# Kernel optimization log

Hardware: AMD Instinct MI355X
Metric: run time of the kernel (lower is better)

Reference implementation:

```python
import jax, jax.numpy as jnp
import numpy as np

B, TQ, TK, D, R, H = 4, 2048, 2048, 1024, 64, 512
TAU_BASE, ASTRO_DECAY = 1.0, 0.95


def setup_inputs() -> dict:
    key = jax.random.key(0)
    ks = jax.random.split(key, 20)
    xav = lambda k, din, dout: jax.random.uniform(k, (din, dout), jnp.float32, -1.0, 1.0) * np.sqrt(6.0 / (din + dout))
    inp = {
        'q_in': jax.random.normal(ks[0], (B, TQ, D), jnp.float32),
        'k_in': jax.random.normal(ks[1], (B, TK, D), jnp.float32),
        'v_in': jax.random.normal(ks[2], (B, TK, D), jnp.float32),
        'astrocyte_state': jnp.zeros((B,), jnp.float32),
        'Wq': xav(ks[3], D, D), 'bq': jnp.zeros((D,), jnp.float32),
        'Wk': xav(ks[4], D, D), 'bk': jnp.zeros((D,), jnp.float32),
        'Wv': xav(ks[5], D, D), 'bv': jnp.zeros((D,), jnp.float32),
        'Wo': xav(ks[6], D, D), 'bo': jnp.zeros((D,), jnp.float32),
        # orthonormal role rows (R <= D): QR of a random D x R matrix, rows = Q^T
        'role_matrix': jnp.linalg.qr(jax.random.normal(ks[7], (D, R), jnp.float32))[0].T,
        'Wr1': xav(ks[8], D, H), 'br1': jnp.zeros((H,), jnp.float32),
        'Wr2': xav(ks[9], H, R),
        'astro_scale': jnp.ones((1,), jnp.float32),
    }
    return inp


def _l2norm(x, axis=-1, eps=1e-12):
    return x / jnp.clip(jnp.linalg.norm(x, axis=axis, keepdims=True), eps)


def _bind_vectors(a, b):
    # holographic (circular-convolution) binding via FFT along feature dim
    n = a.shape[-1]
    return jnp.fft.irfft(jnp.fft.rfft(a, axis=-1) * jnp.fft.rfft(b, axis=-1), n=n, axis=-1)


def _compute_surprise(Q):
    # per-token surprise: RMS-normalized L2 magnitude of projected queries -> (B, T_q)
    return jnp.linalg.norm(Q, axis=-1) / np.sqrt(Q.shape[-1])


def reference(q_in, k_in, v_in, astrocyte_state, Wq, bq, Wk, bk, Wv, bv, Wo, bo,
              role_matrix, Wr1, br1, Wr2, astro_scale):
    Q = q_in @ Wq + bq                      # (B,TQ,D)
    K = k_in @ Wk + bk                      # (B,TK,D)
    V = v_in @ Wv + bv                      # (B,TK,D)

    role_mat_norm = _l2norm(role_matrix)    # (R,D)
    role_logits = jax.nn.relu(K @ Wr1 + br1) @ Wr2          # (B,TK,R)
    role_weights = jax.nn.softmax(role_logits, axis=-1)
    role_vecs = role_weights @ role_mat_norm                 # (B,TK,D)
    K_bound = _bind_vectors(K, role_vecs)                    # (B,TK,D)

    surprise = _compute_surprise(Q)                          # (B,TQ)
    mean_surprise = surprise.mean(axis=-1)                   # (B,)
    new_state = ASTRO_DECAY * astrocyte_state + (1.0 - ASTRO_DECAY) * mean_surprise
    tau_eff = TAU_BASE * jnp.clip(1.0 + astro_scale * new_state, 0.001)[:, None, None]

    q_n = _l2norm(Q)
    k_n = _l2norm(K_bound)
    cos_sim = jnp.einsum('bqd,bkd->bqk', q_n, k_n)           # (B,TQ,TK)
    x = (cos_sim + 1.0) * 0.5
    scores = jnp.clip(1.0 - tau_eff * (1.0 - x) ** 2, 0.0)   # Epanechnikov kernel
    attn = scores / jnp.clip(scores.sum(axis=-1, keepdims=True), 1e-9)
    context = jnp.einsum('bqk,bkd->bqd', attn, V)
    output = context @ Wo + bo
    return output, new_state
```

## Files before the change

### kernel.cpp

```cpp
#include <hip/hip_runtime.h>
#include <stdint.h>


#define Bq 4
#define Tq 2048
#define Dd 1024
#define NT 8192
#define Hh 512
#define Rr_ 64
#define FQ 1024

typedef unsigned short ushort_t;
typedef short s16x8 __attribute__((ext_vector_type(8)));
typedef float floatx4 __attribute__((ext_vector_type(4)));

__device__ __forceinline__ float b2f(ushort_t s) {
  unsigned u = (unsigned)s << 16;
  return __builtin_bit_cast(float, u);
}
__device__ __forceinline__ ushort_t f2b(float f) {
  unsigned u = __builtin_bit_cast(unsigned, f);
  unsigned r = (u + 0x7fffu + ((u >> 16) & 1u)) >> 16;
  return (ushort_t)r;
}

__device__ __forceinline__ void load_lds16(const void* g, void* l) {
  __builtin_amdgcn_global_load_lds((__attribute__((address_space(1))) void*)(g),
                                   (__attribute__((address_space(3))) void*)(l),
                                   16, 0, 0);
}

__device__ __forceinline__ void xcd_swizzle(int& bx, int& by, int& bz) {
  const int gx = gridDim.x, gy = gridDim.y, gz = gridDim.z;
  const int nwg = gx * gy * gz;
  const int orig = (bz * gy + by) * gx + bx;
  const int q = nwg >> 3, r = nwg & 7;
  const int x = orig & 7, i = orig >> 3;
  const int wg = (x < r ? x * (q + 1) : r * (q + 1) + (x - r) * q) + i;
  bx = wg % gx;
  const int t = wg / gx;
  by = t % gy;
  bz = t / gy;
}

struct GOp {
  const ushort_t* A; const ushort_t* Bt;
  float* C; ushort_t* Cbf;
  const float* bias_col; const float* bias_row;
  const float* rmul; const float* cmul; const float* tau;
  float* rowsum;
  int rmulStride, cmulStride, rsStride, rsMode;
  int K, lda, ldb, ldc, flags;
  long long sA, sB, sC;
  int gx, gy, blkStart, pad;
};
struct GB { GOp op[4]; int nOps; int totBlk; };

__global__ __launch_bounds__(512, 2) void gemm256m(GB gb) {
  __shared__ __align__(16) ushort_t lds[2][2][2][256][32];

  int bid = blockIdx.x;
  {
    const int nwg = gb.totBlk;
    const int q = nwg >> 3, r = nwg & 7;
    const int x = bid & 7, i = bid >> 3;
    bid = (x < r ? x * (q + 1) : r * (q + 1) + (x - r) * q) + i;
  }
  int oi = 0;
#pragma unroll
  for (int k = 1; k < 4; k++)
    if (k < gb.nOps && bid >= gb.op[k].blkStart) oi = k;
  const GOp o = gb.op[oi];
  const int local = bid - o.blkStart;
  const int bx = local % o.gx;
  const int tt_ = local / o.gx;
  const int by = tt_ % o.gy;
  const int bz = tt_ / o.gy;

  const ushort_t* Ab = o.A + (size_t)bz * o.sA;
  const ushort_t* Bb = o.Bt + (size_t)bz * o.sB;
  const int tm   = by * 256;
  const int tn   = bx * 256;
  const int tid  = threadIdx.x;
  const int wave = tid >> 6;
  const int lane = tid & 63;
  const int wm   = wave >> 2;
  const int wn   = wave & 3;

  const int s_r  = lane >> 2;
  const int s_cg = (((lane & 3) - (s_r >> 1)) & 3);
  const int f_r  = lane & 15;
  const int f_p  = ((((lane >> 4) + (f_r >> 1)) & 3) << 3);

  const int lda = o.lda, ldb = o.ldb;
  const int NTILES = o.K >> 6;

  floatx4 acc[8][4] = {};

#define STAGE256(tt, g, sl)                                                     \
  do {                                                                          \
    const int mat_ = (g) & 1, h_ = (g) >> 1;                                    \
    const ushort_t* src_ = mat_ ? Bb : Ab;                                      \
    const int ld_ = mat_ ? ldb : lda;                                           \
    const int tb_ = mat_ ? tn : tm;                                             \
    const int kofs_ = (tt) * 64 + h_ * 32 + s_cg * 8;                           \
    _Pragma("unroll")                                                           \
    for (int j_ = 0; j_ < 2; j_++) {                                            \
      const int slab_ = wave * 2 + j_;                                          \
      const ushort_t* gp_ = src_ + (size_t)(tb_ + slab_ * 16 + s_r) * ld_ + kofs_; \
      load_lds16(gp_, (void*)&lds[sl][mat_][h_][slab_ * 16][0]);                \
    }                                                                           \
  } while (0)

  STAGE256(0, 0, 0);
  STAGE256(0, 1, 0);
  STAGE256(0, 2, 0);
  STAGE256(0, 3, 0);
  STAGE256(1, 0, 1);
  STAGE256(1, 1, 1);
  asm volatile("s_waitcnt vmcnt(4)" ::: "memory");
  __builtin_amdgcn_s_barrier();

  for (int t = 0; t < NTILES; t++) {
    const int sl  = t & 1;
    const int sl1 = sl ^ 1;
    const int t1  = (t + 1 < NTILES) ? t + 1 : t;
    const int t2  = (t + 2 < NTILES) ? t + 2 : t;
    s16x8 a[8], b[4];

#pragma unroll
    for (int m = 0; m < 8; m++)
      a[m] = *(const s16x8*)&lds[sl][0][0][wm * 128 + m * 16 + f_r][f_p];
#pragma unroll
    for (int n = 0; n < 4; n++)
      b[n] = *(const s16x8*)&lds[sl][1][0][wn * 64 + n * 16 + f_r][f_p];
    STAGE256(t1, 2, sl1);
    __builtin_amdgcn_s_barrier();
    __builtin_amdgcn_s_setprio(1);
#pragma unroll
    for (int m = 0; m < 8; m++)
#pragma unroll
      for (int n = 0; n < 2; n++)
        acc[m][n] = __builtin_amdgcn_mfma_f32_16x16x32_bf16(a[m], b[n], acc[m][n], 0, 0, 0);
    __builtin_amdgcn_s_setprio(0);
    __builtin_amdgcn_s_barrier();

    STAGE256(t1, 3, sl1);
    __builtin_amdgcn_s_barrier();
    __builtin_amdgcn_s_setprio(1);
#pragma unroll
    for (int m = 0; m < 8; m++)
#pragma unroll
      for (int n = 2; n < 4; n++)
        acc[m][n] = __builtin_amdgcn_mfma_f32_16x16x32_bf16(a[m], b[n], acc[m][n], 0, 0, 0);
    __builtin_amdgcn_s_setprio(0);
    __builtin_amdgcn_s_barrier();

#pragma unroll
    for (int m = 0; m < 8; m++)
      a[m] = *(const s16x8*)&lds[sl][0][1][wm * 128 + m * 16 + f_r][f_p];
#pragma unroll
    for (int n = 0; n < 4; n++)
      b[n] = *(const s16x8*)&lds[sl][1][1][wn * 64 + n * 16 + f_r][f_p];
    STAGE256(t2, 0, sl);
    __builtin_amdgcn_s_barrier();
    __builtin_amdgcn_s_setprio(1);
#pragma unroll
    for (int m = 0; m < 8; m++)
#pragma unroll
      for (int n = 0; n < 2; n++)
        acc[m][n] = __builtin_amdgcn_mfma_f32_16x16x32_bf16(a[m], b[n], acc[m][n], 0, 0, 0);
    __builtin_amdgcn_s_setprio(0);
    __builtin_amdgcn_s_barrier();

    STAGE256(t2, 1, sl);
    __builtin_amdgcn_s_barrier();
    __builtin_amdgcn_s_setprio(1);
#pragma unroll
    for (int m = 0; m < 8; m++)
#pragma unroll
      for (int n = 2; n < 4; n++)
        acc[m][n] = __builtin_amdgcn_mfma_f32_16x16x32_bf16(a[m], b[n], acc[m][n], 0, 0, 0);
    __builtin_amdgcn_s_setprio(0);
    asm volatile("s_waitcnt vmcnt(4)" ::: "memory");
    __builtin_amdgcn_s_barrier();
  }
#undef STAGE256

  const float tv = o.tau ? o.tau[bz] : 0.f;
  float*   Cp  = o.C   ? o.C   + (size_t)bz * o.sC : nullptr;
  ushort_t* Cb = o.Cbf ? o.Cbf + (size_t)bz * o.sC : nullptr;
  float bcv[4], cmv[4];
#pragma unroll
  for (int n = 0; n < 4; n++) {
    const int col = tn + wn * 64 + n * 16 + (lane & 15);
    bcv[n] = o.bias_col ? o.bias_col[col] : 0.f;
    cmv[n] = o.cmul ? o.cmul[(size_t)bz * o.cmulStride + col] : 1.f;
  }
#pragma unroll
  for (int m = 0; m < 8; m++) {
#pragma unroll
    for (int r = 0; r < 4; r++) {
      const int row = tm + wm * 128 + m * 16 + (lane >> 4) * 4 + r;
      const float rm = o.rmul ? o.rmul[(size_t)bz * o.rmulStride + row] : 1.f;
      const float br = o.bias_row ? o.bias_row[row] : 0.f;
      float rsum = 0.f;
#pragma unroll
      for (int n = 0; n < 4; n++) {
        const int col = tn + wn * 64 + n * 16 + (lane & 15);
        float v;
        if (o.flags & 2) {
          v = acc[m][n][r] * (rm * cmv[n]) + bcv[n] + br;
        } else {
          v = (acc[m][n][r] + bcv[n] + br) * (rm * cmv[n]);
        }
        if (o.flags & 1) v = fmaxf(v, 0.f);
        if (o.tau) { float d = 1.0f - v; v = fmaxf(1.0f - tv * 0.25f * d * d, 0.f); }
        rsum += (o.rsMode == 2) ? v * v : v;
        if (Cp) Cp[(size_t)row * o.ldc + col] = v;
        if (Cb) Cb[(size_t)row * o.ldc + col] = f2b(v);
      }
      if (o.rsMode == 1 || o.rsMode == 2) {
        rsum += __shfl_xor(rsum, 1);
        rsum += __shfl_xor(rsum, 2);
        rsum += __shfl_xor(rsum, 4);
        rsum += __shfl_xor(rsum, 8);
        if ((lane & 15) == 0)
          atomicAdd(&o.rowsum[(size_t)bz * o.rsStride + row], rsum);
      }
    }
  }
}

__global__ __launch_bounds__(256) void gemm_bt(
    const ushort_t* __restrict__ A, const ushort_t* __restrict__ Bt,
    float* __restrict__ C, ushort_t* __restrict__ Cbf,
    const float* __restrict__ bias_col, const float* __restrict__ bias_row,
    const float* __restrict__ rmul, int rmulStride,
    const float* __restrict__ cmul, int cmulStride,
    const float* __restrict__ tau,
    float* __restrict__ rowsum, int rsStride, int rsMode,
    int K, int lda, int ldb, int ldc,
    long long sA, long long sB, long long sC, int flags)
{
  __shared__ __align__(16) ushort_t As[128 * 32];
  __shared__ __align__(16) ushort_t Bs[128 * 32];

  int bx = blockIdx.x, by = blockIdx.y, bz = blockIdx.z;
  xcd_swizzle(bx, by, bz);
  const ushort_t* Ab = A + (size_t)bz * sA;
  const ushort_t* Bb = Bt + (size_t)bz * sB;
  const int tm   = by * 128;
  const int tn   = bx * 128;
  const int tid  = threadIdx.x;
  const int wave = tid >> 6;
  const int lane = tid & 63;
  const int wm   = (wave & 1) << 6;
  const int wn   = (wave >> 1) << 6;
  const int sr   = lane >> 2;
  const int cp   = lane & 3;
  const int sc   = (((cp - (sr >> 1)) & 3) << 3);
  const int fr   = lane & 15;
  const int fk   = ((((lane >> 4) + (fr >> 1)) & 3) << 3);

  floatx4 acc[4][4] = {};

  for (int k0 = 0; k0 < K; k0 += 32) {
    {
      const ushort_t* gA0 = Ab + (size_t)(tm + wave * 16 + sr) * lda + (k0 + sc);
      const ushort_t* gA1 = gA0 + (size_t)64 * lda;
      char* lA = (char*)As + wave * 1024;
      load_lds16(gA0, lA);
      load_lds16(gA1, lA + 4096);
      const ushort_t* gB0 = Bb + (size_t)(tn + wave * 16 + sr) * ldb + (k0 + sc);
      const ushort_t* gB1 = gB0 + (size_t)64 * ldb;
      char* lB = (char*)Bs + wave * 1024;
      load_lds16(gB0, lB);
      load_lds16(gB1, lB + 4096);
    }
    __syncthreads();
    s16x8 af[4], bfv[4];
#pragma unroll
    for (int i = 0; i < 4; i++)
      af[i] = *(const s16x8*)&As[(wm + i * 16 + fr) * 32 + fk];
#pragma unroll
    for (int j = 0; j < 4; j++)
      bfv[j] = *(const s16x8*)&Bs[(wn + j * 16 + fr) * 32 + fk];
#pragma unroll
    for (int i = 0; i < 4; i++)
#pragma unroll
      for (int j = 0; j < 4; j++)
        acc[i][j] = __builtin_amdgcn_mfma_f32_16x16x32_bf16(af[i], bfv[j], acc[i][j], 0, 0, 0);
    __syncthreads();
  }

  const float tv = tau ? tau[bz] : 0.f;
  float*   Cp  = C   ? C   + (size_t)bz * sC : nullptr;
  ushort_t* Cb = Cbf ? Cbf + (size_t)bz * sC : nullptr;
  float bcv[4], cmv[4];
#pragma unroll
  for (int j = 0; j < 4; j++) {
    const int col = tn + wn + j * 16 + (lane & 15);
    bcv[j] = bias_col ? bias_col[col] : 0.f;
    cmv[j] = cmul ? cmul[(size_t)bz * cmulStride + col] : 1.f;
  }
#pragma unroll
  for (int i = 0; i < 4; i++) {
#pragma unroll
    for (int r = 0; r < 4; r++) {
      const int row = tm + wm + i * 16 + (lane >> 4) * 4 + r;
      const float rm = rmul ? rmul[(size_t)bz * rmulStride + row] : 1.f;
      const float br = bias_row ? bias_row[row] : 0.f;
      float rsum = 0.f;
#pragma unroll
      for (int j = 0; j < 4; j++) {
        const int col = tn + wn + j * 16 + (lane & 15);
        float v;
        if (flags & 2) {
          v = acc[i][j][r] * (rm * cmv[j]) + bcv[j] + br;
        } else {
          v = (acc[i][j][r] + bcv[j] + br) * (rm * cmv[j]);
        }
        if (flags & 1) v = fmaxf(v, 0.f);
        if (tau) { float d = 1.0f - v; v = fmaxf(1.0f - tv * 0.25f * d * d, 0.f); }
        rsum += (rsMode == 2) ? v * v : v;
        if (Cp) Cp[(size_t)row * ldc + col] = v;
        if (Cb) Cb[(size_t)row * ldc + col] = f2b(v);
      }
      if (rsMode == 1 || rsMode == 2) {
        rsum += __shfl_xor(rsum, 1);
        rsum += __shfl_xor(rsum, 2);
        rsum += __shfl_xor(rsum, 4);
        rsum += __shfl_xor(rsum, 8);
        if ((lane & 15) == 0)
          atomicAdd(&rowsum[(size_t)bz * rsStride + row], rsum);
      }
    }
  }
}

struct P3 { const ushort_t* A[3]; const ushort_t* Bt[3]; ushort_t* C[3]; int M[3]; };

__global__ __launch_bounds__(256) void prep3(P3 p) {
  __shared__ __align__(16) ushort_t As[128 * 32];
  __shared__ __align__(16) ushort_t Bs[128 * 32];
  const int z  = blockIdx.z;
  const int tm = blockIdx.y * 128;
  if (tm >= p.M[z]) return;
  const ushort_t* Ab = p.A[z];
  const ushort_t* Bb = p.Bt[z];
  ushort_t*       Cc = p.C[z];
  const int tn   = blockIdx.x * 128;
  const int tid  = threadIdx.x;
  const int wave = tid >> 6;
  const int lane = tid & 63;
  const int wm   = (wave & 1) << 6;
  const int wn   = (wave >> 1) << 6;
  const int sr   = lane >> 2;
  const int cp   = lane & 3;
  const int sc   = (((cp - (sr >> 1)) & 3) << 3);
  const int fr   = lane & 15;
  const int fk   = ((((lane >> 4) + (fr >> 1)) & 3) << 3);

  floatx4 acc[4][4] = {};

  for (int k0 = 0; k0 < Dd; k0 += 32) {
    {
      const ushort_t* gA0 = Ab + (size_t)(tm + wave * 16 + sr) * Dd + (k0 + sc);
      const ushort_t* gA1 = gA0 + (size_t)64 * Dd;
      char* lA = (char*)As + wave * 1024;
      load_lds16(gA0, lA);
      load_lds16(gA1, lA + 4096);
      const ushort_t* gB0 = Bb + (size_t)(tn + wave * 16 + sr) * Dd + (k0 + sc);
      const ushort_t* gB1 = gB0 + (size_t)64 * Dd;
      char* lB = (char*)Bs + wave * 1024;
      load_lds16(gB0, lB);
      load_lds16(gB1, lB + 4096);
    }
    __syncthreads();
    s16x8 af[4], bfv[4];
#pragma unroll
    for (int i = 0; i < 4; i++)
      af[i] = *(const s16x8*)&As[(wm + i * 16 + fr) * 32 + fk];
#pragma unroll
    for (int j = 0; j < 4; j++)
      bfv[j] = *(const s16x8*)&Bs[(wn + j * 16 + fr) * 32 + fk];
#pragma unroll
    for (int i = 0; i < 4; i++)
#pragma unroll
      for (int j = 0; j < 4; j++)
        acc[i][j] = __builtin_amdgcn_mfma_f32_16x16x32_bf16(af[i], bfv[j], acc[i][j], 0, 0, 0);
    __syncthreads();
  }

#pragma unroll
  for (int i = 0; i < 4; i++)
#pragma unroll
    for (int r = 0; r < 4; r++) {
      const int row = tm + wm + i * 16 + (lane >> 4) * 4 + r;
#pragma unroll
      for (int j = 0; j < 4; j++) {
        const int col = tn + wn + j * 16 + (lane & 15);
        Cc[(size_t)row * Dd + col] = f2b(acc[i][j][r]);
      }
    }
}

__global__ __launch_bounds__(256) void castbf(const float* __restrict__ in,
                                              ushort_t* __restrict__ out, int n4) {
  int i = blockIdx.x * 256 + threadIdx.x;
  if (i >= n4) return;
  float4 v = ((const float4*)in)[i];
  ushort4 o;
  o.x = f2b(v.x); o.y = f2b(v.y); o.z = f2b(v.z); o.w = f2b(v.w);
  ((ushort4*)out)[i] = o;
}

struct TC4 { const float* in[4]; ushort_t* out[4]; };
__global__ __launch_bounds__(256) void tcast4(TC4 p) {
  __shared__ float t[32][33];
  int z = blockIdx.z;
  const float* in = p.in[z];
  ushort_t* out = p.out[z];
  int r0 = blockIdx.x * 32, c0 = blockIdx.y * 32;
  int x = threadIdx.x, y = threadIdx.y;
  for (int dy = 0; dy < 32; dy += 8)
    t[y + dy][x] = in[(size_t)(r0 + y + dy) * 1024 + c0 + x];
  __syncthreads();
  for (int dy = 0; dy < 32; dy += 8)
    out[(size_t)(c0 + y + dy) * 1024 + r0 + x] = f2b(t[x][y + dy]);
}

__global__ __launch_bounds__(256) void tcast(const float* __restrict__ in,
                                             ushort_t* __restrict__ out,
                                             int RrN, int Cc, int Cp) {
  __shared__ float t[32][33];
  int r0 = blockIdx.x * 32, c0 = blockIdx.y * 32;
  int x = threadIdx.x, y = threadIdx.y;
  for (int dy = 0; dy < 32; dy += 8) {
    int r = r0 + y + dy, c = c0 + x;
    t[y + dy][x] = (c < Cc) ? in[(size_t)r * Cc + c] : 0.f;
  }
  __syncthreads();
  for (int dy = 0; dy < 32; dy += 8) {
    int c = c0 + y + dy, r = r0 + x;
    if (c < Cp) out[(size_t)c * RrN + r] = f2b(t[x][y + dy]);
  }
}

__global__ __launch_bounds__(256) void rolenorm(const float* __restrict__ rm,
                                                ushort_t* __restrict__ rmn) {
  int r = blockIdx.x, tid = threadIdx.x;
  float4 v = ((const float4*)(rm + (size_t)r * 1024))[tid];
  float s = v.x * v.x + v.y * v.y + v.z * v.z + v.w * v.w;
#pragma unroll
  for (int m = 1; m < 64; m <<= 1) s += __shfl_xor(s, m);
  __shared__ float red[6];
  if ((tid & 63) == 0) red[tid >> 6] = s;
  __syncthreads();
  if (tid == 0) red[4] = 1.f / fmaxf(sqrtf(red[0] + red[1] + red[2] + red[3]), 1e-12f);
  __syncthreads();
  float inv = red[4];
  ushort4 o;
  o.x = f2b(v.x * inv); o.y = f2b(v.y * inv); o.z = f2b(v.z * inv); o.w = f2b(v.w * inv);
  ((ushort4*)(rmn + (size_t)r * 1024))[tid] = o;
}

__global__ __launch_bounds__(256) void rfn_kernel(const ushort_t* __restrict__ rmn,
                                                  const ushort_t* __restrict__ ftab,
                                                  ushort_t* __restrict__ RFnT) {
  int f = blockIdx.x;
  int t = threadIdx.x;
  int r = t >> 2, part = t & 3;
  const ushort_t* fr = ftab + (size_t)f * 1024 + part * 256;
  const ushort_t* rr = rmn + (size_t)r * 1024 + part * 256;
  float s = 0.f;
#pragma unroll 4
  for (int i = 0; i < 32; i++) {
    s16x8 a = *(const s16x8*)(fr + i * 8);
    s16x8 b = *(const s16x8*)(rr + i * 8);
#pragma unroll
    for (int j = 0; j < 8; j++) s += b2f((ushort_t)a[j]) * b2f((ushort_t)b[j]);
  }
  s += __shfl_xor(s, 1);
  s += __shfl_xor(s, 2);
  if (part == 0) RFnT[(size_t)f * 128 + r] = f2b(s);
}

__global__ __launch_bounds__(64) void foldbk(const ushort_t* __restrict__ ftab,
                                             const float* __restrict__ bk,
                                             float* __restrict__ bkF) {
  int j = blockIdx.x, lane = threadIdx.x;
  const ushort_t* row = ftab + (size_t)j * 1024 + lane * 16;
  const float* bp = bk + lane * 16;
  float s = 0.f;
#pragma unroll
  for (int i = 0; i < 2; i++) {
    s16x8 a = *(const s16x8*)(row + i * 8);
#pragma unroll
    for (int e = 0; e < 8; e++) s += b2f((ushort_t)a[e]) * bp[i * 8 + e];
  }
#pragma unroll
  for (int m = 1; m < 64; m <<= 1) s += __shfl_xor(s, m);
  if (lane == 0) bkF[j] = s;
}

__global__ __launch_bounds__(256) void foldbh(const float* __restrict__ Wr1,
                                              const float* __restrict__ bk,
                                              const float* __restrict__ br1,
                                              float* __restrict__ bh) {
  int h = blockIdx.x * 256 + threadIdx.x;
  float s = br1[h];
  for (int d = 0; d < 1024; d++) s += bk[d] * Wr1[(size_t)d * Hh + h];
  bh[h] = s;
}

__global__ __launch_bounds__(256) void foldbvo(const float* __restrict__ Wo,
                                               const float* __restrict__ bv,
                                               const float* __restrict__ bo,
                                               float* __restrict__ bvo) {
  int d = blockIdx.x * 256 + threadIdx.x;
  float s = bo[d];
  for (int e = 0; e < 1024; e++) s += bv[e] * Wo[(size_t)e * 1024 + d];
  bvo[d] = s;
}

__global__ __launch_bounds__(256) void invnorm_surprise(const float* __restrict__ ssq,
                                                        float* __restrict__ invn,
                                                        float* __restrict__ ssum) {
  int row = blockIdx.x * 256 + threadIdx.x;
  float nrm = sqrtf(ssq[row]);
  invn[row] = 1.f / fmaxf(nrm, 1e-12f);
  float t = nrm;
#pragma unroll
  for (int m = 1; m < 64; m <<= 1) t += __shfl_xor(t, m);
  if ((threadIdx.x & 63) == 0) atomicAdd(&ssum[row >> 11], t);
}

__global__ __launch_bounds__(256) void invnorm(const float* __restrict__ ssq,
                                               float* __restrict__ invn) {
  int row = blockIdx.x * 256 + threadIdx.x;
  invn[row] = 1.f / fmaxf(sqrtf(ssq[row]), 1e-12f);
}

__global__ __launch_bounds__(256) void invrowsum(const float* __restrict__ rs,
                                                 float* __restrict__ inv) {
  int row = blockIdx.x * 256 + threadIdx.x;
  inv[row] = 1.f / fmaxf(rs[row], 1e-9f);
}

__global__ void finalize_astro(const float* __restrict__ ssum, const float* __restrict__ astro,
                               const float* __restrict__ ascale, float* __restrict__ tau,
                               float* __restrict__ outTail) {
  int b = threadIdx.x;
  if (b < Bq) {
    float mean = ssum[b] * (1.f / (32.f * 2048.f));
    float ns = 0.95f * astro[b] + 0.05f * mean;
    tau[b] = fmaxf(1.f + ascale[0] * ns, 0.001f);
    outTail[b] = ns;
  }
}

__global__ __launch_bounds__(256) void softmax64(const float* __restrict__ logits,
                                                 ushort_t* __restrict__ out) {
  int row = blockIdx.x * 4 + (threadIdx.x >> 6);
  int lane = threadIdx.x & 63;
  float x = logits[(size_t)row * 128 + lane];
  float m = x;
#pragma unroll
  for (int s = 1; s < 64; s <<= 1) m = fmaxf(m, __shfl_xor(m, s));
  float e = expf(x - m);
  float sum = e;
#pragma unroll
  for (int s = 1; s < 64; s <<= 1) sum += __shfl_xor(sum, s);
  out[(size_t)row * 64 + lane] = f2b(e / sum);
}

__global__ __launch_bounds__(256) void gen_ftab(ushort_t* __restrict__ ftab) {
  const float TW = 6.283185307179586f / 1024.f;
  int idx = blockIdx.x * 256 + threadIdx.x;
  int j = idx >> 10, k = idx & 1023;
  int f = j <= 512 ? j : j - 512;
  float th = (float)((f * k) & 1023) * TW;
  float sv, cv; sincosf(th, &sv, &cv);
  ftab[idx] = f2b(j <= 512 ? cv : -sv);
}

__global__ __launch_bounds__(256) void gen_itab(ushort_t* __restrict__ itab) {
  const float TW = 6.283185307179586f / 1024.f;
  int idx = blockIdx.x * 256 + threadIdx.x;
  int n = idx >> 10, j = idx & 1023;
  float v;
  if (j <= 512) {
    float w = (j == 0 || j == 512) ? (1.f / 1024.f) : (2.f / 1024.f);
    float th = (float)((j * n) & 1023) * TW;
    float sv, cv; sincosf(th, &sv, &cv);
    v = w * cv;
  } else {
    int f = j - 512;
    float th = (float)((f * n) & 1023) * TW;
    float sv, cv; sincosf(th, &sv, &cv);
    v = -(2.f / 1024.f) * sv;
  }
  itab[idx] = f2b(v);
}

__global__ __launch_bounds__(256) void fftmul(const ushort_t* __restrict__ KF,
                                              const ushort_t* __restrict__ RF,
                                              ushort_t* __restrict__ P) {
  int idx = blockIdx.x * 256 + threadIdx.x;
  int t = idx >> 9;
  int j = idx & 511;
  size_t base = (size_t)t * FQ;
  if (j == 0) {
    P[base]       = f2b(b2f(KF[base]) * b2f(RF[base]));
    P[base + 512] = f2b(b2f(KF[base + 512]) * b2f(RF[base + 512]));
  } else {
    float a = b2f(KF[base + j]), b = b2f(KF[base + 512 + j]);
    float c = b2f(RF[base + j]), d = b2f(RF[base + 512 + j]);
    P[base + j]       = f2b(a * c - b * d);
    P[base + 512 + j] = f2b(a * d + b * c);
  }
}

static constexpr size_t OFF_RS    = 0;
static constexpr size_t OFF_SSQQ  = 32768;
static constexpr size_t OFF_SSQK  = 65536;
static constexpr size_t OFF_INVQ  = 98304;
static constexpr size_t OFF_INVK  = 131072;
static constexpr size_t OFF_INVRS = 163840;
static constexpr size_t OFF_SSUM  = 196608;
static constexpr size_t OFF_TAU   = 196864;
static constexpr size_t OFF_WQT   = 197120;
static constexpr size_t OFF_WKB   = OFF_WQT  + 2097152;
static constexpr size_t OFF_WVB   = OFF_WKB  + 2097152;
static constexpr size_t OFF_WOT   = OFF_WVB  + 2097152;
static constexpr size_t OFF_WR1T  = OFF_WOT  + 2097152;
static constexpr size_t OFF_WR2T  = OFF_WR1T + 1048576;
static constexpr size_t OFF_RMN   = OFF_WR2T + 131072;
static constexpr size_t OFF_FTAB  = OFF_RMN  + 131072;
static constexpr size_t OFF_ITAB  = OFF_FTAB + 2097152;
static constexpr size_t OFF_RFNT  = OFF_ITAB + 2097152;
static constexpr size_t OFF_B1    = OFF_RFNT + 262144;
static constexpr size_t OFF_B2    = OFF_B1   + 16777216;
static constexpr size_t OFF_B3    = OFF_B2   + 16777216;
static constexpr size_t OFF_B4    = OFF_B3   + 16777216;
static constexpr size_t OFF_B5    = OFF_B4   + 16777216;
static constexpr size_t OFF_B6    = OFF_B5   + 16777216;
static constexpr size_t OFF_B7    = OFF_B6   + 16777216;
static constexpr size_t OFF_HID   = OFF_B7   + 16777216;
static constexpr size_t OFF_LOGI  = OFF_HID  + 8388608;
static constexpr size_t OFF_RW    = OFF_LOGI + 4194304;
static constexpr size_t OFF_SB    = OFF_RW   + 1048576;
static constexpr size_t WS_NEEDED = OFF_SB   + 33554432;
static constexpr size_t OFF_WKF   = OFF_B6;
static constexpr size_t OFF_WOV   = OFF_B6 + 2097152;
static constexpr size_t OFF_WKR1  = OFF_B6 + 4194304;
static constexpr size_t OFF_BKF   = OFF_B6 + 5242880;
static constexpr size_t OFF_BH    = OFF_B6 + 5247232;
static constexpr size_t OFF_BVO   = OFF_B6 + 5249536;

static inline void launch_gemm(hipStream_t s, const ushort_t* A, const ushort_t* Bt,
                               float* Cf, ushort_t* Cb,
                               const float* bias_col, const float* bias_row,
                               const float* rmul, int rmulStride,
                               const float* cmul, int cmulStride,
                               const float* tau, float* rowsum, int rsStride, int rsMode,
                               int M, int N, int K, int lda, int ldb, int ldc,
                               long long sA, long long sB, long long sC, int Z, int flags) {
  dim3 g(N / 128, M / 128, Z), b(256);
  gemm_bt<<<g, b, 0, s>>>(A, Bt, Cf, Cb, bias_col, bias_row, rmul, rmulStride,
                          cmul, cmulStride, tau, rowsum, rsStride, rsMode,
                          K, lda, ldb, ldc, sA, sB, sC, flags);
}

static inline GOp mkop(const ushort_t* A, const ushort_t* Bt, float* Cf, ushort_t* Cb,
                       const float* bias_col, const float* rmul, int rmulStride,
                       const float* cmul, int cmulStride, const float* tau,
                       float* rowsum, int rsStride, int rsMode,
                       int M, int N, int K, int lda, int ldb, int ldc,
                       long long sA, long long sB, long long sC, int flags, int blkStart) {
  GOp o;
  o.A = A; o.Bt = Bt; o.C = Cf; o.Cbf = Cb;
  o.bias_col = bias_col; o.bias_row = nullptr;
  o.rmul = rmul; o.cmul = cmul; o.tau = tau; o.rowsum = rowsum;
  o.rmulStride = rmulStride; o.cmulStride = cmulStride;
  o.rsStride = rsStride; o.rsMode = rsMode;
  o.K = K; o.lda = lda; o.ldb = ldb; o.ldc = ldc; o.flags = flags;
  o.sA = sA; o.sB = sB; o.sC = sC;
  o.gx = N / 256; o.gy = M / 256; o.blkStart = blkStart; o.pad = 0;
  return o;
}

extern "C" void kernel_launch(void* const* d_in, const int* in_sizes, int n_in,
                              void* d_out, int out_size, void* d_ws, size_t ws_size,
                              hipStream_t stream) {
  (void)in_sizes; (void)n_in; (void)out_size;
  if (ws_size < WS_NEEDED) return;

  const float* q_in  = (const float*)d_in[0];
  const float* k_in  = (const float*)d_in[1];
  const float* v_in  = (const float*)d_in[2];
  const float* astro = (const float*)d_in[3];
  const float* Wq    = (const float*)d_in[4];
  const float* bq    = (const float*)d_in[5];
  const float* Wk    = (const float*)d_in[6];
  const float* bk    = (const float*)d_in[7];
  const float* Wv    = (const float*)d_in[8];
  const float* bv    = (const float*)d_in[9];
  const float* Wo    = (const float*)d_in[10];
  const float* bo    = (const float*)d_in[11];
  const float* roleM = (const float*)d_in[12];
  const float* Wr1   = (const float*)d_in[13];
  const float* br1   = (const float*)d_in[14];
  const float* Wr2   = (const float*)d_in[15];
  const float* ascl  = (const float*)d_in[16];

  char* ws = (char*)d_ws;
  float*    rowsumS = (float*)(ws + OFF_RS);
  float*    ssqQ    = (float*)(ws + OFF_SSQQ);
  float*    ssqK    = (float*)(ws + OFF_SSQK);
  float*    invQ    = (float*)(ws + OFF_INVQ);
  float*    invK    = (float*)(ws + OFF_INVK);
  float*    invRS   = (float*)(ws + OFF_INVRS);
  float*    ssum    = (float*)(ws + OFF_SSUM);
  float*    tau     = (float*)(ws + OFF_TAU);
  ushort_t* WqT  = (ushort_t*)(ws + OFF_WQT);
  ushort_t* Wkb  = (ushort_t*)(ws + OFF_WKB);
  ushort_t* Wvb  = (ushort_t*)(ws + OFF_WVB);
  ushort_t* WoT  = (ushort_t*)(ws + OFF_WOT);
  ushort_t* Wr1T = (ushort_t*)(ws + OFF_WR1T);
  ushort_t* Wr2T = (ushort_t*)(ws + OFF_WR2T);
  ushort_t* rmn  = (ushort_t*)(ws + OFF_RMN);
  ushort_t* FTab = (ushort_t*)(ws + OFF_FTAB);
  ushort_t* ITab = (ushort_t*)(ws + OFF_ITAB);
  ushort_t* RFnT = (ushort_t*)(ws + OFF_RFNT);
  ushort_t* qbf  = (ushort_t*)(ws + OFF_B1);
  ushort_t* kbraw= (ushort_t*)(ws + OFF_B1);
  ushort_t* kinb = (ushort_t*)(ws + OFF_B2);
  ushort_t* RF   = (ushort_t*)(ws + OFF_B2);
  ushort_t* vinb = (ushort_t*)(ws + OFF_B3);
  ushort_t* Pb   = (ushort_t*)(ws + OFF_B3);
  ushort_t* qraw = (ushort_t*)(ws + OFF_B4);
  ushort_t* KF   = (ushort_t*)(ws + OFF_B5);
  ushort_t* WkF  = (ushort_t*)(ws + OFF_WKF);
  ushort_t* Wov  = (ushort_t*)(ws + OFF_WOV);
  ushort_t* WkR1 = (ushort_t*)(ws + OFF_WKR1);
  float*    bkF  = (float*)(ws + OFF_BKF);
  float*    bh   = (float*)(ws + OFF_BH);
  float*    bvo  = (float*)(ws + OFF_BVO);
  ushort_t* vT   = (ushort_t*)(ws + OFF_B7);
  ushort_t* hid  = (ushort_t*)(ws + OFF_HID);
  float*    logi = (float*)(ws + OFF_LOGI);
  ushort_t* rw   = (ushort_t*)(ws + OFF_RW);
  ushort_t* Sb   = (ushort_t*)(ws + OFF_SB);
  float*    out  = (float*)d_out;

  hipMemsetAsync(ws, 0, OFF_SSUM + 256, stream);

  TC4 tc4;
  tc4.in[0] = Wq; tc4.out[0] = WqT;
  tc4.in[1] = Wo; tc4.out[1] = WoT;
  tc4.in[2] = Wq; tc4.out[2] = WqT;
  tc4.in[3] = Wq; tc4.out[3] = WqT;
  tcast4<<<dim3(32, 32, 2), dim3(32, 8), 0, stream>>>(tc4);
  castbf<<<1024, 256, 0, stream>>>(Wk, Wkb, 262144);
  castbf<<<1024, 256, 0, stream>>>(Wv, Wvb, 262144);
  tcast<<<dim3(32, 16), dim3(32, 8), 0, stream>>>(Wr1, Wr1T, 1024, 512, 512);
  tcast<<<dim3(16, 4),  dim3(32, 8), 0, stream>>>(Wr2, Wr2T, 512, 64, 128);
  rolenorm<<<64, 256, 0, stream>>>(roleM, rmn);
  gen_ftab<<<(FQ * 1024) / 256, 256, 0, stream>>>(FTab);
  gen_itab<<<(1024 * FQ) / 256, 256, 0, stream>>>(ITab);
  rfn_kernel<<<FQ, 256, 0, stream>>>(rmn, FTab, RFnT);

  P3 p3;
  p3.A[0] = FTab; p3.Bt[0] = Wkb; p3.C[0] = WkF;  p3.M[0] = 1024;
  p3.A[1] = WoT;  p3.Bt[1] = Wvb; p3.C[1] = Wov;  p3.M[1] = 1024;
  p3.A[2] = Wr1T; p3.Bt[2] = Wkb; p3.C[2] = WkR1; p3.M[2] = 512;
  prep3<<<dim3(8, 8, 3), 256, 0, stream>>>(p3);
  foldbk<<<1024, 64, 0, stream>>>(FTab, bk, bkF);
  foldbh<<<Hh / 256, 256, 0, stream>>>(Wr1, bk, br1, bh);
  foldbvo<<<Dd / 256, 256, 0, stream>>>(Wo, bv, bo, bvo);

  castbf<<<8192, 256, 0, stream>>>(q_in, qbf, NT * Dd / 4);
  castbf<<<8192, 256, 0, stream>>>(k_in, kinb, NT * Dd / 4);
  castbf<<<8192, 256, 0, stream>>>(v_in, vinb, NT * Dd / 4);

  {
    GB gb;
    gb.op[0] = mkop(qbf, WqT, nullptr, qraw, bq, nullptr, 0, nullptr, 0, nullptr,
                    ssqQ, 0, 2, NT, Dd, Dd, Dd, Dd, Dd, 0, 0, 0, 0, 0);
    gb.op[1] = mkop(kinb, WkF, nullptr, KF, bkF, nullptr, 0, nullptr, 0, nullptr,
                    nullptr, 0, 0, NT, FQ, Dd, Dd, Dd, FQ, 0, 0, 0, 0, 128);
    gb.op[2] = mkop(Wov, vinb, nullptr, vT, nullptr, nullptr, 0, nullptr, 0, nullptr,
                    nullptr, 0, 0, Dd, NT, Dd, Dd, Dd, NT, 0, 0, 0, 0, 256);
    gb.op[3] = mkop(kinb, WkR1, nullptr, hid, bh, nullptr, 0, nullptr, 0, nullptr,
                    nullptr, 0, 0, NT, Hh, Dd, Dd, Dd, Hh, 0, 0, 0, 1 , 384);
    gb.nOps = 4; gb.totBlk = 448;
    gemm256m<<<dim3(448), dim3(512), 0, stream>>>(gb);
  }
  invnorm_surprise<<<NT / 256, 256, 0, stream>>>(ssqQ, invQ, ssum);
  finalize_astro<<<1, 64, 0, stream>>>(ssum, astro, ascl, tau, out + (size_t)NT * Dd);

  launch_gemm(stream, hid, Wr2T, logi, nullptr, nullptr, nullptr,
              nullptr, 0, nullptr, 0, nullptr, nullptr, 0, 0,
              NT, 128, Hh, Hh, Hh, 128, 0, 0, 0, 1, 0);
  softmax64<<<NT / 4, 256, 0, stream>>>(logi, rw);
  launch_gemm(stream, rw, RFnT, nullptr, RF, nullptr, nullptr,
              nullptr, 0, nullptr, 0, nullptr, nullptr, 0, 0,
              NT, FQ, Rr_, Rr_, 128, FQ, 0, 0, 0, 1, 0);

  fftmul<<<(NT * 512) / 256, 256, 0, stream>>>(KF, RF, Pb);
  launch_gemm(stream, Pb, ITab, nullptr, kbraw, nullptr, nullptr,
              nullptr, 0, nullptr, 0, nullptr, ssqK, 0, 2,
              NT, Dd, FQ, FQ, FQ, Dd, 0, 0, 0, 1, 0);
  invnorm<<<NT / 256, 256, 0, stream>>>(ssqK, invK);

  {
    GB gb;
    GOp o = mkop(qraw, kbraw, nullptr, Sb, nullptr, invQ, Tq, invK, Tq, tau,
                 rowsumS, Tq, 1, Tq, Tq, Dd, Dd, Dd, Tq,
                 (long long)Tq * Dd, (long long)Tq * Dd, (long long)Tq * Tq, 0, 0);
    gb.op[0] = o; gb.op[1] = o; gb.op[2] = o; gb.op[3] = o;
    gb.nOps = 1; gb.totBlk = 256;
    gemm256m<<<dim3(256), dim3(512), 0, stream>>>(gb);
  }
  invrowsum<<<NT / 256, 256, 0, stream>>>(rowsumS, invRS);

  launch_gemm(stream, Sb, vT, out, nullptr, bvo, nullptr,
              invRS, Tq, nullptr, 0, nullptr, nullptr, 0, 0,
              Tq, Dd, Tq, Tq, NT, Dd,
              (long long)Tq * Tq, (long long)Tq, (long long)Tq * Dd, Bq, 2 );
}
```

Baseline: 707.3 us.

## Use 128-tile multi-op GEMM for projections, fuse input casts, derive itab from ftab

```diff
diff --git a/kernel.cpp b/kernel.cpp
--- a/kernel.cpp
+++ b/kernel.cpp
@@ -55,6 +55,120 @@
   int gx, gy, blkStart, pad;
 };
 struct GB { GOp op[4]; int nOps; int totBlk; };
+
+__global__ __launch_bounds__(256) void gemm_btm(GB gb) {
+  __shared__ __align__(16) ushort_t As[128 * 32];
+  __shared__ __align__(16) ushort_t Bs[128 * 32];
+
+  int bid = blockIdx.x;
+  {
+    const int nwg = gb.totBlk;
+    const int q = nwg >> 3, r = nwg & 7;
+    const int x = bid & 7, i = bid >> 3;
+    bid = (x < r ? x * (q + 1) : r * (q + 1) + (x - r) * q) + i;
+  }
+  int oi = 0;
+#pragma unroll
+  for (int k = 1; k < 4; k++)
+    if (k < gb.nOps && bid >= gb.op[k].blkStart) oi = k;
+  const GOp o = gb.op[oi];
+  const int local = bid - o.blkStart;
+  const int bx = local % o.gx;
+  const int tt_ = local / o.gx;
+  const int by = tt_ % o.gy;
+  const int bz = tt_ / o.gy;
+
+  const ushort_t* Ab = o.A + (size_t)bz * o.sA;
+  const ushort_t* Bb = o.Bt + (size_t)bz * o.sB;
+  const int lda = o.lda, ldb = o.ldb;
+  const int tm   = by * 128;
+  const int tn   = bx * 128;
+  const int tid  = threadIdx.x;
+  const int wave = tid >> 6;
+  const int lane = tid & 63;
+  const int wm   = (wave & 1) << 6;
+  const int wn   = (wave >> 1) << 6;
+  const int sr   = lane >> 2;
+  const int cp   = lane & 3;
+  const int sc   = (((cp - (sr >> 1)) & 3) << 3);
+  const int fr   = lane & 15;
+  const int fk   = ((((lane >> 4) + (fr >> 1)) & 3) << 3);
+
+  floatx4 acc[4][4] = {};
+
+  for (int k0 = 0; k0 < o.K; k0 += 32) {
+    {
+      const ushort_t* gA0 = Ab + (size_t)(tm + wave * 16 + sr) * lda + (k0 + sc);
+      const ushort_t* gA1 = gA0 + (size_t)64 * lda;
+      char* lA = (char*)As + wave * 1024;
+      load_lds16(gA0, lA);
+      load_lds16(gA1, lA + 4096);
+      const ushort_t* gB0 = Bb + (size_t)(tn + wave * 16 + sr) * ldb + (k0 + sc);
+      const ushort_t* gB1 = gB0 + (size_t)64 * ldb;
+      char* lB = (char*)Bs + wave * 1024;
+      load_lds16(gB0, lB);
+      load_lds16(gB1, lB + 4096);
+    }
+    __syncthreads();
+    s16x8 af[4], bfv[4];
+#pragma unroll
+    for (int i = 0; i < 4; i++)
+      af[i] = *(const s16x8*)&As[(wm + i * 16 + fr) * 32 + fk];
+#pragma unroll
+    for (int j = 0; j < 4; j++)
+      bfv[j] = *(const s16x8*)&Bs[(wn + j * 16 + fr) * 32 + fk];
+#pragma unroll
+    for (int i = 0; i < 4; i++)
+#pragma unroll
+      for (int j = 0; j < 4; j++)
+        acc[i][j] = __builtin_amdgcn_mfma_f32_16x16x32_bf16(af[i], bfv[j], acc[i][j], 0, 0, 0);
+    __syncthreads();
+  }
+
+  const float tv = o.tau ? o.tau[bz] : 0.f;
+  float*   Cp  = o.C   ? o.C   + (size_t)bz * o.sC : nullptr;
+  ushort_t* Cb = o.Cbf ? o.Cbf + (size_t)bz * o.sC : nullptr;
+  float bcv[4], cmv[4];
+#pragma unroll
+  for (int j = 0; j < 4; j++) {
+    const int col = tn + wn + j * 16 + (lane & 15);
+    bcv[j] = o.bias_col ? o.bias_col[col] : 0.f;
+    cmv[j] = o.cmul ? o.cmul[(size_t)bz * o.cmulStride + col] : 1.f;
+  }
+#pragma unroll
+  for (int i = 0; i < 4; i++) {
+#pragma unroll
+    for (int r = 0; r < 4; r++) {
+      const int row = tm + wm + i * 16 + (lane >> 4) * 4 + r;
+      const float rm = o.rmul ? o.rmul[(size_t)bz * o.rmulStride + row] : 1.f;
+      const float br = o.bias_row ? o.bias_row[row] : 0.f;
+      float rsum = 0.f;
+#pragma unroll
+      for (int j = 0; j < 4; j++) {
+        const int col = tn + wn + j * 16 + (lane & 15);
+        float v;
+        if (o.flags & 2) {
+          v = acc[i][j][r] * (rm * cmv[j]) + bcv[j] + br;
+        } else {
+          v = (acc[i][j][r] + bcv[j] + br) * (rm * cmv[j]);
+        }
+        if (o.flags & 1) v = fmaxf(v, 0.f);
+        if (o.tau) { float d = 1.0f - v; v = fmaxf(1.0f - tv * 0.25f * d * d, 0.f); }
+        rsum += (o.rsMode == 2) ? v * v : v;
+        if (Cp) Cp[(size_t)row * o.ldc + col] = v;
+        if (Cb) Cb[(size_t)row * o.ldc + col] = f2b(v);
+      }
+      if (o.rsMode == 1 || o.rsMode == 2) {
+        rsum += __shfl_xor(rsum, 1);
+        rsum += __shfl_xor(rsum, 2);
+        rsum += __shfl_xor(rsum, 4);
+        rsum += __shfl_xor(rsum, 8);
+        if ((lane & 15) == 0)
+          atomicAdd(&o.rowsum[(size_t)bz * o.rsStride + row], rsum);
+      }
+    }
+  }
+}
 
 __global__ __launch_bounds__(512, 2) void gemm256m(GB gb) {
   __shared__ __align__(16) ushort_t lds[2][2][2][256][32];
@@ -416,6 +530,16 @@
   ((ushort4*)out)[i] = o;
 }
 
+struct C3 { const float* in[3]; ushort_t* out[3]; };
+__global__ __launch_bounds__(256) void castbf3(C3 p) {
+  int z = blockIdx.y;
+  int i = blockIdx.x * 256 + threadIdx.x;
+  float4 v = ((const float4*)p.in[z])[i];
+  ushort4 o;
+  o.x = f2b(v.x); o.y = f2b(v.y); o.z = f2b(v.z); o.w = f2b(v.w);
+  ((ushort4*)p.out[z])[i] = o;
+}
+
 struct TC4 { const float* in[4]; ushort_t* out[4]; };
 __global__ __launch_bounds__(256) void tcast4(TC4 p) {
   __shared__ float t[32][33];
@@ -586,23 +710,19 @@
   ftab[idx] = f2b(j <= 512 ? cv : -sv);
 }
 
-__global__ __launch_bounds__(256) void gen_itab(ushort_t* __restrict__ itab) {
-  const float TW = 6.283185307179586f / 1024.f;
-  int idx = blockIdx.x * 256 + threadIdx.x;
-  int n = idx >> 10, j = idx & 1023;
-  float v;
-  if (j <= 512) {
-    float w = (j == 0 || j == 512) ? (1.f / 1024.f) : (2.f / 1024.f);
-    float th = (float)((j * n) & 1023) * TW;
-    float sv, cv; sincosf(th, &sv, &cv);
-    v = w * cv;
-  } else {
-    int f = j - 512;
-    float th = (float)((f * n) & 1023) * TW;
-    float sv, cv; sincosf(th, &sv, &cv);
-    v = -(2.f / 1024.f) * sv;
-  }
-  itab[idx] = f2b(v);
+__global__ __launch_bounds__(256) void titab(const ushort_t* __restrict__ ftab,
+                                             ushort_t* __restrict__ itab) {
+  __shared__ float t[32][33];
+  int j0 = blockIdx.x * 32, n0 = blockIdx.y * 32;
+  int x = threadIdx.x, y = threadIdx.y;
+  for (int dy = 0; dy < 32; dy += 8) {
+    int j = j0 + y + dy;
+    float s = (j == 0 || j == 512) ? (1.f / 1024.f) : (2.f / 1024.f);
+    t[y + dy][x] = b2f(ftab[(size_t)j * 1024 + n0 + x]) * s;
+  }
+  __syncthreads();
+  for (int dy = 0; dy < 32; dy += 8)
+    itab[(size_t)(n0 + y + dy) * 1024 + j0 + x] = f2b(t[x][y + dy]);
 }
 
 __global__ __launch_bounds__(256) void fftmul(const ushort_t* __restrict__ KF,
@@ -679,7 +799,8 @@
                        const float* cmul, int cmulStride, const float* tau,
                        float* rowsum, int rsStride, int rsMode,
                        int M, int N, int K, int lda, int ldb, int ldc,
-                       long long sA, long long sB, long long sC, int flags, int blkStart) {
+                       long long sA, long long sB, long long sC, int flags,
+                       int blkStart, int tile) {
   GOp o;
   o.A = A; o.Bt = Bt; o.C = Cf; o.Cbf = Cb;
   o.bias_col = bias_col; o.bias_row = nullptr;
@@ -688,7 +809,7 @@
   o.rsStride = rsStride; o.rsMode = rsMode;
   o.K = K; o.lda = lda; o.ldb = ldb; o.ldc = ldc; o.flags = flags;
   o.sA = sA; o.sB = sB; o.sC = sC;
-  o.gx = N / 256; o.gy = M / 256; o.blkStart = blkStart; o.pad = 0;
+  o.gx = N / tile; o.gy = M / tile; o.blkStart = blkStart; o.pad = 0;
   return o;
 }
 
@@ -770,7 +891,7 @@
   tcast<<<dim3(16, 4),  dim3(32, 8), 0, stream>>>(Wr2, Wr2T, 512, 64, 128);
   rolenorm<<<64, 256, 0, stream>>>(roleM, rmn);
   gen_ftab<<<(FQ * 1024) / 256, 256, 0, stream>>>(FTab);
-  gen_itab<<<(1024 * FQ) / 256, 256, 0, stream>>>(ITab);
+  titab<<<dim3(32, 32), dim3(32, 8), 0, stream>>>(FTab, ITab);
   rfn_kernel<<<FQ, 256, 0, stream>>>(rmn, FTab, RFnT);
 
   P3 p3;
@@ -782,22 +903,24 @@
   foldbh<<<Hh / 256, 256, 0, stream>>>(Wr1, bk, br1, bh);
   foldbvo<<<Dd / 256, 256, 0, stream>>>(Wo, bv, bo, bvo);
 
-  castbf<<<8192, 256, 0, stream>>>(q_in, qbf, NT * Dd / 4);
-  castbf<<<8192, 256, 0, stream>>>(k_in, kinb, NT * Dd / 4);
-  castbf<<<8192, 256, 0, stream>>>(v_in, vinb, NT * Dd / 4);
+  C3 c3;
+  c3.in[0] = q_in; c3.out[0] = qbf;
+  c3.in[1] = k_in; c3.out[1] = kinb;
+  c3.in[2] = v_in; c3.out[2] = vinb;
+  castbf3<<<dim3(8192, 3), 256, 0, stream>>>(c3);
 
   {
     GB gb;
     gb.op[0] = mkop(qbf, WqT, nullptr, qraw, bq, nullptr, 0, nullptr, 0, nullptr,
-                    ssqQ, 0, 2, NT, Dd, Dd, Dd, Dd, Dd, 0, 0, 0, 0, 0);
+                    ssqQ, 0, 2, NT, Dd, Dd, Dd, Dd, Dd, 0, 0, 0, 0, 0, 128);
     gb.op[1] = mkop(kinb, WkF, nullptr, KF, bkF, nullptr, 0, nullptr, 0, nullptr,
-                    nullptr, 0, 0, NT, FQ, Dd, Dd, Dd, FQ, 0, 0, 0, 0, 128);
+                    nullptr, 0, 0, NT, FQ, Dd, Dd, Dd, FQ, 0, 0, 0, 0, 512, 128);
     gb.op[2] = mkop(Wov, vinb, nullptr, vT, nullptr, nullptr, 0, nullptr, 0, nullptr,
-                    nullptr, 0, 0, Dd, NT, Dd, Dd, Dd, NT, 0, 0, 0, 0, 256);
+                    nullptr, 0, 0, Dd, NT, Dd, Dd, Dd, NT, 0, 0, 0, 0, 1024, 128);
     gb.op[3] = mkop(kinb, WkR1, nullptr, hid, bh, nullptr, 0, nullptr, 0, nullptr,
-                    nullptr, 0, 0, NT, Hh, Dd, Dd, Dd, Hh, 0, 0, 0, 1 , 384);
-    gb.nOps = 4; gb.totBlk = 448;
-    gemm256m<<<dim3(448), dim3(512), 0, stream>>>(gb);
+                    nullptr, 0, 0, NT, Hh, Dd, Dd, Dd, Hh, 0, 0, 0, 1 , 1536, 128);
+    gb.nOps = 4; gb.totBlk = 1792;
+    gemm_btm<<<dim3(1792), dim3(256), 0, stream>>>(gb);
   }
   invnorm_surprise<<<NT / 256, 256, 0, stream>>>(ssqQ, invQ, ssum);
   finalize_astro<<<1, 64, 0, stream>>>(ssum, astro, ascl, tau, out + (size_t)NT * Dd);
@@ -820,7 +943,7 @@
     GB gb;
     GOp o = mkop(qraw, kbraw, nullptr, Sb, nullptr, invQ, Tq, invK, Tq, tau,
                  rowsumS, Tq, 1, Tq, Tq, Dd, Dd, Dd, Tq,
-                 (long long)Tq * Dd, (long long)Tq * Dd, (long long)Tq * Tq, 0, 0);
+                 (long long)Tq * Dd, (long long)Tq * Dd, (long long)Tq * Tq, 0, 0, 256);
     gb.op[0] = o; gb.op[1] = o; gb.op[2] = o; gb.op[3] = o;
     gb.nOps = 1; gb.totBlk = 256;
     gemm256m<<<dim3(256), dim3(512), 0, stream>>>(gb);
```

Result: no change. 696.4 us (-1.5%).
